# Kernel tuning notes

Measured on AMD Instinct MI355X. Metric: run time of the kernel, lower is better.

The kernel has to match this reference:

```python
import jax, jax.numpy as jnp
import numpy as np

B, Hh, Ww, D = 16, 74, 74, 768   # batch, patch-grid h, patch-grid w, feature dim
NH, NO = 8, 16                    # humans / objects per image
N_REL = 117                       # HOI relation classes


def _make_boxes(key, n):
    # valid boxes: x2 > x1, y2 > y1, all within [0, 74]
    k1, k2, k3, k4 = jax.random.split(key, 4)
    x1 = jax.random.randint(k1, (B, n), 0, Ww - 16)
    y1 = jax.random.randint(k2, (B, n), 0, Hh - 16)
    bw = jax.random.randint(k3, (B, n), 2, 16)
    bh = jax.random.randint(k4, (B, n), 2, 16)
    return jnp.stack([x1, y1, x1 + bw, y1 + bh], axis=-1).astype(jnp.int32)


def setup_inputs() -> dict:
    key = jax.random.key(0)
    ks = jax.random.split(key, 8)
    features = jax.random.normal(ks[0], (B, Hh, Ww, D), dtype=jnp.float32)
    human_boxes = _make_boxes(ks[1], NH)
    obj_boxes = _make_boxes(ks[2], NO)
    s = 0.02
    W1 = jax.random.normal(ks[3], (2 * D, 512), dtype=jnp.float32) * s
    b1 = jnp.zeros((512,), jnp.float32)
    W2 = jax.random.normal(ks[4], (512, 256), dtype=jnp.float32) * s
    b2 = jnp.zeros((256,), jnp.float32)
    W3 = jax.random.normal(ks[5], (256, N_REL), dtype=jnp.float32) * s
    b3 = jnp.zeros((N_REL,), jnp.float32)
    return {"features": features, "human_boxes": human_boxes, "obj_boxes": obj_boxes,
            "W1": W1, "b1": b1, "W2": W2, "b2": b2, "W3": W3, "b3": b3}


def _roi_mean(feats, boxes):
    # feats: [h, w, D]; boxes: [N, 4] int (x1, y1, x2, y2) in patch coords.
    # Mean of feats[y1:y2, x1:x2] via a summed-area table (vectorized, one pass).
    integ = jnp.cumsum(jnp.cumsum(feats, axis=0), axis=1)
    integ = jnp.pad(integ, ((1, 0), (1, 0), (0, 0)))  # [h+1, w+1, D]
    x1, y1, x2, y2 = boxes[:, 0], boxes[:, 1], boxes[:, 2], boxes[:, 3]
    s = integ[y2, x2] - integ[y1, x2] - integ[y2, x1] + integ[y1, x1]  # [N, D]
    area = ((y2 - y1) * (x2 - x1)).astype(feats.dtype)[:, None]
    return s / area


def reference(features, human_boxes, obj_boxes, W1, b1, W2, b2, W3, b3):
    hf = jax.vmap(_roi_mean)(features, human_boxes)  # [B, NH, D]
    of = jax.vmap(_roi_mean)(features, obj_boxes)    # [B, NO, D]
    # pairwise concat: for every (human, object) pair -> [B, NH, NO, 2D]
    pairs = jnp.concatenate([
        jnp.broadcast_to(hf[:, :, None, :], (B, NH, NO, D)),
        jnp.broadcast_to(of[:, None, :, :], (B, NH, NO, D)),
    ], axis=-1).reshape(B * NH * NO, 2 * D)
    h = jax.nn.relu(pairs @ W1 + b1)
    h = jax.nn.relu(h @ W2 + b2)
    return h @ W3 + b3  # [B*NH*NO, 117] relation scores
```

## Files before the change

kernel.cpp:

```cpp
#include <hip/hip_runtime.h>

#define BB   16
#define HH   74
#define WW   74
#define DD   768
#define NHh  8
#define NOo  16
#define NREL 117
#define NKQ  8
#define KCH  96
#define ABSTRIDE (384 * 512)

#define FMA4(A, s, W) \
    A.x = fmaf((s), (W).x, A.x); A.y = fmaf((s), (W).y, A.y); \
    A.z = fmaf((s), (W).z, A.z); A.w = fmaf((s), (W).w, A.w);


__global__ __launch_bounds__(512, 6) void roi_gemm1_kernel(const float* __restrict__ feats,
                                                           const int* __restrict__ hboxes,
                                                           const int* __restrict__ oboxes,
                                                           const float* __restrict__ W1,
                                                           float* __restrict__ AB)
{
    __shared__ __align__(16) float part[15][4][KCH];
    __shared__ __align__(16) float xs[4][KCH];
    __shared__ __align__(16) float red[2][4][512];
    int r0 = blockIdx.x * 4;
    int kq = blockIdx.y;
    int t = threadIdx.x;

    if (t < 360) {
        int c4 = t % 24;
        int s  = t / 24;
        for (int r = 0; r < 4; ++r) {
            int row = r0 + r;
            const int* box = (row < 128) ? (hboxes + row * 4) : (oboxes + (row - 128) * 4);
            int x1 = box[0], y1 = box[1], x2 = box[2], y2 = box[3];
            if (s < y2 - y1) {
                int b = (row < 128) ? (row >> 3) : ((row - 128) >> 4);
                int y = y1 + s;
                const float4* rp = (const float4*)(feats + (size_t)((b * HH + y) * WW) * DD + kq * KCH) + c4;
                float4 a0 = make_float4(0.f, 0.f, 0.f, 0.f);
                float4 a1 = make_float4(0.f, 0.f, 0.f, 0.f);
                float4 a2 = make_float4(0.f, 0.f, 0.f, 0.f);
                float4 a3 = make_float4(0.f, 0.f, 0.f, 0.f);
                int x = x1;
                for (; x + 3 < x2; x += 4) {
                    float4 v0 = rp[(size_t)(x + 0) * 192];
                    float4 v1 = rp[(size_t)(x + 1) * 192];
                    float4 v2 = rp[(size_t)(x + 2) * 192];
                    float4 v3 = rp[(size_t)(x + 3) * 192];
                    a0.x += v0.x; a0.y += v0.y; a0.z += v0.z; a0.w += v0.w;
                    a1.x += v1.x; a1.y += v1.y; a1.z += v1.z; a1.w += v1.w;
                    a2.x += v2.x; a2.y += v2.y; a2.z += v2.z; a2.w += v2.w;
                    a3.x += v3.x; a3.y += v3.y; a3.z += v3.z; a3.w += v3.w;
                }
                for (; x < x2; ++x) {
                    float4 v0 = rp[(size_t)x * 192];
                    a0.x += v0.x; a0.y += v0.y; a0.z += v0.z; a0.w += v0.w;
                }
                a0.x += a1.x + a2.x + a3.x;
                a0.y += a1.y + a2.y + a3.y;
                a0.z += a1.z + a2.z + a3.z;
                a0.w += a1.w + a2.w + a3.w;
                *(float4*)&part[s][r][c4 * 4] = a0;
            }
        }
    }
    __syncthreads();

    for (int idx = t; idx < 4 * KCH; idx += 512) {
        int r = idx / KCH;
        int k = idx - r * KCH;
        int row = r0 + r;
        const int* box = (row < 128) ? (hboxes + row * 4) : (oboxes + (row - 128) * 4);
        int bh = box[3] - box[1];
        float inv_area = 1.0f / (float)(bh * (box[2] - box[0]));
        float ssum = 0.f;
        for (int s = 0; s < bh; ++s) ssum += part[s][r][k];
        xs[r][k] = ssum * inv_area;
    }
    __syncthreads();

    if (t < 256) {
        int c  = t & 127;
        int kh = t >> 7;
        int kb = kh * 48;
        const float* W1p = W1 + ((size_t)(((r0 < 128) ? 0 : DD) + kq * KCH + kb)) * 512 + 4 * c;

        float4 a[4];
#pragma unroll
        for (int r = 0; r < 4; ++r) a[r] = make_float4(0.f, 0.f, 0.f, 0.f);

        for (int kk = 0; kk < 48; kk += 8) {
            float4 w[8];
#pragma unroll
            for (int u = 0; u < 8; ++u) w[u] = *(const float4*)(W1p + (size_t)(kk + u) * 512);
#pragma unroll
            for (int r = 0; r < 4; ++r) {
                float4 x0 = *(const float4*)&xs[r][kb + kk];
                float4 x1 = *(const float4*)&xs[r][kb + kk + 4];
                float xv[8] = {x0.x, x0.y, x0.z, x0.w, x1.x, x1.y, x1.z, x1.w};
#pragma unroll
                for (int u = 0; u < 8; ++u) { FMA4(a[r], xv[u], w[u]); }
            }
        }
#pragma unroll
        for (int r = 0; r < 4; ++r) *(float4*)&red[kh][r][4 * c] = a[r];
    }
    __syncthreads();

    float* ABq = AB + (size_t)kq * ABSTRIDE;
    for (int idx = t; idx < 4 * 512; idx += 512) {
        int r = idx >> 9;
        int cc = idx & 511;
        ABq[(size_t)(r0 + r) * 512 + cc] = red[0][r][cc] + red[1][r][cc];
    }
}

__global__ __launch_bounds__(1024, 4) void mlp_kernel(const float* __restrict__ AB,
                                                      const float* __restrict__ b1,
                                                      const float* __restrict__ W2,
                                                      const float* __restrict__ b2,
                                                      const float* __restrict__ W3,
                                                      const float* __restrict__ b3,
                                                      float* __restrict__ out)
{
    __shared__ __align__(16) float h1[8][512];
    __shared__ __align__(16) float red[8][8][256];
    __shared__ __align__(16) float h2[8][256];
    int p0 = blockIdx.x * 8;
    int t = threadIdx.x;

    {
        int r  = t >> 7;
        int k4 = t & 127;
        int p = p0 + r;
        int rowA = p >> 4;
        int rowB = 128 + (p >> 7) * 16 + (p & 15);
        float4 v = ((const float4*)b1)[k4];
#pragma unroll
        for (int q = 0; q < NKQ; ++q) {
            float4 av = ((const float4*)(AB + (size_t)q * ABSTRIDE + (size_t)rowA * 512))[k4];
            float4 bv = ((const float4*)(AB + (size_t)q * ABSTRIDE + (size_t)rowB * 512))[k4];
            v.x += av.x + bv.x; v.y += av.y + bv.y;
            v.z += av.z + bv.z; v.w += av.w + bv.w;
        }
        v.x = v.x > 0.f ? v.x : 0.f; v.y = v.y > 0.f ? v.y : 0.f;
        v.z = v.z > 0.f ? v.z : 0.f; v.w = v.w > 0.f ? v.w : 0.f;
        *(float4*)&h1[r][k4 * 4] = v;
    }
    __syncthreads();

    {
        int c   = t & 63;
        int kq2 = (t >> 6) & 7;
        int rh  = t >> 9;
        int kbase = kq2 * 64;
        const float* W2p = W2 + (size_t)kbase * 256 + 4 * c;
        float4 a[4];
#pragma unroll
        for (int r = 0; r < 4; ++r) a[r] = make_float4(0.f, 0.f, 0.f, 0.f);

        for (int kk = 0; kk < 64; kk += 8) {
            float4 w[8];
#pragma unroll
            for (int u = 0; u < 8; ++u) w[u] = *(const float4*)(W2p + (size_t)(kk + u) * 256);
#pragma unroll
            for (int r = 0; r < 4; ++r) {
                float4 x0 = *(const float4*)&h1[rh * 4 + r][kbase + kk];
                float4 x1 = *(const float4*)&h1[rh * 4 + r][kbase + kk + 4];
                float xv[8] = {x0.x, x0.y, x0.z, x0.w, x1.x, x1.y, x1.z, x1.w};
#pragma unroll
                for (int u = 0; u < 8; ++u) { FMA4(a[r], xv[u], w[u]); }
            }
        }
#pragma unroll
        for (int r = 0; r < 4; ++r) *(float4*)&red[kq2][rh * 4 + r][4 * c] = a[r];
    }
    __syncthreads();

    for (int idx = t; idx < 8 * 256; idx += 1024) {
        int r = idx >> 8;
        int cc = idx & 255;
        float s = b2[cc];
#pragma unroll
        for (int q = 0; q < 8; ++q) s += red[q][r][cc];
        h2[r][cc] = s > 0.f ? s : 0.f;
    }
    __syncthreads();

    float* pr = &red[0][0][0];
    if (t < 8 * NREL) {
        int o = t % NREL;
        int jq = t / NREL;
        float acc[8] = {};
        const float* W3p = W3 + o;
        for (int j = jq * 32; j < jq * 32 + 32; j += 8) {
            float w[8];
#pragma unroll
            for (int u = 0; u < 8; ++u) w[u] = W3p[(size_t)(j + u) * NREL];
#pragma unroll
            for (int r = 0; r < 8; ++r) {
                float4 x0 = *(const float4*)&h2[r][j];
                float4 x1 = *(const float4*)&h2[r][j + 4];
                acc[r] = fmaf(x0.x, w[0], acc[r]); acc[r] = fmaf(x0.y, w[1], acc[r]);
                acc[r] = fmaf(x0.z, w[2], acc[r]); acc[r] = fmaf(x0.w, w[3], acc[r]);
                acc[r] = fmaf(x1.x, w[4], acc[r]); acc[r] = fmaf(x1.y, w[5], acc[r]);
                acc[r] = fmaf(x1.z, w[6], acc[r]); acc[r] = fmaf(x1.w, w[7], acc[r]);
            }
        }
#pragma unroll
        for (int r = 0; r < 8; ++r) pr[(jq * 8 + r) * NREL + o] = acc[r];
    }
    __syncthreads();

    if (t < 8 * NREL) {
        int r = t / NREL;
        int o = t - r * NREL;
        float s = b3[o];
#pragma unroll
        for (int q = 0; q < 8; ++q) s += pr[(q * 8 + r) * NREL + o];
        out[(size_t)(p0 + r) * NREL + o] = s;
    }
}

extern "C" void kernel_launch(void* const* d_in, const int* in_sizes, int n_in,
                              void* d_out, int out_size, void* d_ws, size_t ws_size,
                              hipStream_t stream) {
    const float* feats  = (const float*)d_in[0];
    const int*   hboxes = (const int*)d_in[1];
    const int*   oboxes = (const int*)d_in[2];
    const float* W1     = (const float*)d_in[3];
    const float* b1     = (const float*)d_in[4];
    const float* W2     = (const float*)d_in[5];
    const float* b2     = (const float*)d_in[6];
    const float* W3     = (const float*)d_in[7];
    const float* b3     = (const float*)d_in[8];
    float* out = (float*)d_out;

    float* AB = (float*)d_ws;

    roi_gemm1_kernel<<<dim3(96, NKQ), dim3(512), 0, stream>>>(feats, hboxes, oboxes, W1, AB);
    mlp_kernel<<<dim3(256), dim3(1024), 0, stream>>>(AB, b1, W2, b2, W3, b3, out);
}
```

Measured before the change: 43.84 us.

## Split ROI mean and first GEMM into separate kernels, halve K-split count

The fused ROI-pooling plus first-layer GEMM kernel becomes two kernels. A row-mean kernel has one block per box read all 768 features per pixel and write pooled rows to workspace. A GEMM kernel then multiplies those rows by W1. The K split drops from 8 chunks of 96 to 4 chunks of 192, with all 512 threads doing the GEMM and a 4-way reduction in shared memory. This aims for better-coalesced feature reads, fewer partial sums for the MLP kernel to combine, and better thread use. The cost is an extra kernel launch and a workspace round trip for the pooled features.

```diff
diff --git a/kernel.cpp b/kernel.cpp
--- a/kernel.cpp
+++ b/kernel.cpp
@@ -7,8 +7,8 @@
 #define NHh  8
 #define NOo  16
 #define NREL 117
-#define NKQ  8
-#define KCH  96
+#define NKQ  4
+#define KCH  192
 #define ABSTRIDE (384 * 512)
 
 #define FMA4(A, s, W) \
@@ -16,105 +16,109 @@
     A.z = fmaf((s), (W).z, A.z); A.w = fmaf((s), (W).w, A.w);
 
 
-__global__ __launch_bounds__(512, 6) void roi_gemm1_kernel(const float* __restrict__ feats,
-                                                           const int* __restrict__ hboxes,
-                                                           const int* __restrict__ oboxes,
-                                                           const float* __restrict__ W1,
-                                                           float* __restrict__ AB)
+__global__ __launch_bounds__(768) void rowmean_kernel(const float* __restrict__ feats,
+                                                      const int* __restrict__ hboxes,
+                                                      const int* __restrict__ oboxes,
+                                                      float* __restrict__ X)
 {
-    __shared__ __align__(16) float part[15][4][KCH];
+    __shared__ __align__(16) float part[4][768];
+    int row = blockIdx.x;
+    const int* box = (row < 128) ? (hboxes + row * 4) : (oboxes + (row - 128) * 4);
+    int x1 = box[0], y1 = box[1], x2 = box[2], y2 = box[3];
+    int b = (row < 128) ? (row >> 3) : ((row - 128) >> 4);
+    int t = threadIdx.x;
+    int c4 = t % 192;
+    int s  = t / 192;
+
+    float4 a0 = make_float4(0.f, 0.f, 0.f, 0.f);
+    float4 a1 = make_float4(0.f, 0.f, 0.f, 0.f);
+    float4 a2 = make_float4(0.f, 0.f, 0.f, 0.f);
+    float4 a3 = make_float4(0.f, 0.f, 0.f, 0.f);
+    for (int y = y1 + s; y < y2; y += 4) {
+        const float4* rp = (const float4*)(feats + (size_t)((b * HH + y) * WW) * DD) + c4;
+        int x = x1;
+        for (; x + 3 < x2; x += 4) {
+            float4 v0 = rp[(size_t)(x + 0) * 192];
+            float4 v1 = rp[(size_t)(x + 1) * 192];
+            float4 v2 = rp[(size_t)(x + 2) * 192];
+            float4 v3 = rp[(size_t)(x + 3) * 192];
+            a0.x += v0.x; a0.y += v0.y; a0.z += v0.z; a0.w += v0.w;
+            a1.x += v1.x; a1.y += v1.y; a1.z += v1.z; a1.w += v1.w;
+            a2.x += v2.x; a2.y += v2.y; a2.z += v2.z; a2.w += v2.w;
+            a3.x += v3.x; a3.y += v3.y; a3.z += v3.z; a3.w += v3.w;
+        }
+        for (; x < x2; ++x) {
+            float4 v0 = rp[(size_t)x * 192];
+            a0.x += v0.x; a0.y += v0.y; a0.z += v0.z; a0.w += v0.w;
+        }
+    }
+    a0.x += a1.x + a2.x + a3.x;
+    a0.y += a1.y + a2.y + a3.y;
+    a0.z += a1.z + a2.z + a3.z;
+    a0.w += a1.w + a2.w + a3.w;
+    *(float4*)&part[s][c4 * 4] = a0;
+    __syncthreads();
+
+    float inv_area = 1.0f / (float)((y2 - y1) * (x2 - x1));
+    float v = (part[0][t] + part[1][t] + part[2][t] + part[3][t]) * inv_area;
+    X[(size_t)row * DD + t] = v;
+}
+
+__global__ __launch_bounds__(512) void gemm1_kernel(const float* __restrict__ X,
+                                                    const float* __restrict__ W1,
+                                                    float* __restrict__ AB)
+{
     __shared__ __align__(16) float xs[4][KCH];
-    __shared__ __align__(16) float red[2][4][512];
+    __shared__ __align__(16) float red[4][4][512];
     int r0 = blockIdx.x * 4;
     int kq = blockIdx.y;
     int t = threadIdx.x;
 
-    if (t < 360) {
-        int c4 = t % 24;
-        int s  = t / 24;
-        for (int r = 0; r < 4; ++r) {
-            int row = r0 + r;
-            const int* box = (row < 128) ? (hboxes + row * 4) : (oboxes + (row - 128) * 4);
-            int x1 = box[0], y1 = box[1], x2 = box[2], y2 = box[3];
-            if (s < y2 - y1) {
-                int b = (row < 128) ? (row >> 3) : ((row - 128) >> 4);
-                int y = y1 + s;
-                const float4* rp = (const float4*)(feats + (size_t)((b * HH + y) * WW) * DD + kq * KCH) + c4;
-                float4 a0 = make_float4(0.f, 0.f, 0.f, 0.f);
-                float4 a1 = make_float4(0.f, 0.f, 0.f, 0.f);
-                float4 a2 = make_float4(0.f, 0.f, 0.f, 0.f);
-                float4 a3 = make_float4(0.f, 0.f, 0.f, 0.f);
-                int x = x1;
-                for (; x + 3 < x2; x += 4) {
-                    float4 v0 = rp[(size_t)(x + 0) * 192];
-                    float4 v1 = rp[(size_t)(x + 1) * 192];
-                    float4 v2 = rp[(size_t)(x + 2) * 192];
-                    float4 v3 = rp[(size_t)(x + 3) * 192];
-                    a0.x += v0.x; a0.y += v0.y; a0.z += v0.z; a0.w += v0.w;
-                    a1.x += v1.x; a1.y += v1.y; a1.z += v1.z; a1.w += v1.w;
-                    a2.x += v2.x; a2.y += v2.y; a2.z += v2.z; a2.w += v2.w;
-                    a3.x += v3.x; a3.y += v3.y; a3.z += v3.z; a3.w += v3.w;
-                }
-                for (; x < x2; ++x) {
-                    float4 v0 = rp[(size_t)x * 192];
-                    a0.x += v0.x; a0.y += v0.y; a0.z += v0.z; a0.w += v0.w;
-                }
-                a0.x += a1.x + a2.x + a3.x;
-                a0.y += a1.y + a2.y + a3.y;
-                a0.z += a1.z + a2.z + a3.z;
-                a0.w += a1.w + a2.w + a3.w;
-                *(float4*)&part[s][r][c4 * 4] = a0;
-            }
-        }
-    }
-    __syncthreads();
-
-    for (int idx = t; idx < 4 * KCH; idx += 512) {
+    {
+        int r = t / KCH;
+        int k = t - r * KCH;
+        xs[r][k] = X[(size_t)(r0 + r) * DD + kq * KCH + k];
+    }
+    if (t < 256) {
+        int idx = t + 512;
         int r = idx / KCH;
         int k = idx - r * KCH;
-        int row = r0 + r;
-        const int* box = (row < 128) ? (hboxes + row * 4) : (oboxes + (row - 128) * 4);
-        int bh = box[3] - box[1];
-        float inv_area = 1.0f / (float)(bh * (box[2] - box[0]));
-        float ssum = 0.f;
-        for (int s = 0; s < bh; ++s) ssum += part[s][r][k];
-        xs[r][k] = ssum * inv_area;
-    }
-    __syncthreads();
-
-    if (t < 256) {
-        int c  = t & 127;
-        int kh = t >> 7;
-        int kb = kh * 48;
-        const float* W1p = W1 + ((size_t)(((r0 < 128) ? 0 : DD) + kq * KCH + kb)) * 512 + 4 * c;
-
-        float4 a[4];
-#pragma unroll
-        for (int r = 0; r < 4; ++r) a[r] = make_float4(0.f, 0.f, 0.f, 0.f);
-
-        for (int kk = 0; kk < 48; kk += 8) {
-            float4 w[8];
-#pragma unroll
-            for (int u = 0; u < 8; ++u) w[u] = *(const float4*)(W1p + (size_t)(kk + u) * 512);
-#pragma unroll
-            for (int r = 0; r < 4; ++r) {
-                float4 x0 = *(const float4*)&xs[r][kb + kk];
-                float4 x1 = *(const float4*)&xs[r][kb + kk + 4];
-                float xv[8] = {x0.x, x0.y, x0.z, x0.w, x1.x, x1.y, x1.z, x1.w};
-#pragma unroll
-                for (int u = 0; u < 8; ++u) { FMA4(a[r], xv[u], w[u]); }
-            }
-        }
-#pragma unroll
-        for (int r = 0; r < 4; ++r) *(float4*)&red[kh][r][4 * c] = a[r];
-    }
+        xs[r][k] = X[(size_t)(r0 + r) * DD + kq * KCH + k];
+    }
+    __syncthreads();
+
+    int c  = t & 127;
+    int kh = t >> 7;
+    int kb = kh * 48;
+    const float* W1p = W1 + ((size_t)(((r0 < 128) ? 0 : DD) + kq * KCH + kb)) * 512 + 4 * c;
+
+    float4 a[4];
+#pragma unroll
+    for (int r = 0; r < 4; ++r) a[r] = make_float4(0.f, 0.f, 0.f, 0.f);
+
+    for (int kk = 0; kk < 48; kk += 8) {
+        float4 w[8];
+#pragma unroll
+        for (int u = 0; u < 8; ++u) w[u] = *(const float4*)(W1p + (size_t)(kk + u) * 512);
+#pragma unroll
+        for (int r = 0; r < 4; ++r) {
+            float4 x0 = *(const float4*)&xs[r][kb + kk];
+            float4 x1 = *(const float4*)&xs[r][kb + kk + 4];
+            float xv[8] = {x0.x, x0.y, x0.z, x0.w, x1.x, x1.y, x1.z, x1.w};
+#pragma unroll
+            for (int u = 0; u < 8; ++u) { FMA4(a[r], xv[u], w[u]); }
+        }
+    }
+#pragma unroll
+    for (int r = 0; r < 4; ++r) *(float4*)&red[kh][r][4 * c] = a[r];
     __syncthreads();
 
     float* ABq = AB + (size_t)kq * ABSTRIDE;
     for (int idx = t; idx < 4 * 512; idx += 512) {
         int r = idx >> 9;
         int cc = idx & 511;
-        ABq[(size_t)(r0 + r) * 512 + cc] = red[0][r][cc] + red[1][r][cc];
+        ABq[(size_t)(r0 + r) * 512 + cc] = red[0][r][cc] + red[1][r][cc]
+                                         + red[2][r][cc] + red[3][r][cc];
     }
 }
 
@@ -240,7 +244,9 @@
     float* out = (float*)d_out;
 
     float* AB = (float*)d_ws;
-
-    roi_gemm1_kernel<<<dim3(96, NKQ), dim3(512), 0, stream>>>(feats, hboxes, oboxes, W1, AB);
+    float* X  = AB + (size_t)NKQ * ABSTRIDE;
+
+    rowmean_kernel<<<dim3(384), dim3(768), 0, stream>>>(feats, hboxes, oboxes, X);
+    gemm1_kernel<<<dim3(96, NKQ), dim3(512), 0, stream>>>(X, W1, AB);
     mlp_kernel<<<dim3(256), dim3(1024), 0, stream>>>(AB, b1, W2, b2, W3, b3, out);
 }
```

Result: slower. 49.64 us (+13.3%).

## Process one ROI row per block instead of four in ROI+GEMM1 kernel

Applied to the files above, without the earlier changes.

The fused ROI-mean and first-layer GEMM kernel now handles one box row per block, launching 384×8 blocks instead of 96×8. The GEMM phase uses all 512 threads with a 4-way split over K instead of 256 threads, and the partial sums are reduced from four slices. The aim is more parallelism and better load balance across CUs for the memory-bound box sums. In exchange, each W1 slice is reloaded once per row instead of once per four rows, which raises W1 traffic about fourfold.

```diff
diff --git a/kernel.cpp b/kernel.cpp
--- a/kernel.cpp
+++ b/kernel.cpp
@@ -16,106 +16,89 @@
     A.z = fmaf((s), (W).z, A.z); A.w = fmaf((s), (W).w, A.w);
 
 
-__global__ __launch_bounds__(512, 6) void roi_gemm1_kernel(const float* __restrict__ feats,
-                                                           const int* __restrict__ hboxes,
-                                                           const int* __restrict__ oboxes,
-                                                           const float* __restrict__ W1,
-                                                           float* __restrict__ AB)
+__global__ __launch_bounds__(512) void roi_gemm1_kernel(const float* __restrict__ feats,
+                                                        const int* __restrict__ hboxes,
+                                                        const int* __restrict__ oboxes,
+                                                        const float* __restrict__ W1,
+                                                        float* __restrict__ AB)
 {
-    __shared__ __align__(16) float part[15][4][KCH];
-    __shared__ __align__(16) float xs[4][KCH];
-    __shared__ __align__(16) float red[2][4][512];
-    int r0 = blockIdx.x * 4;
-    int kq = blockIdx.y;
+    __shared__ __align__(16) float part[15][KCH];
+    __shared__ __align__(16) float xs[KCH];
+    __shared__ __align__(16) float red[4][512];
+    int row = blockIdx.x;
+    int kq  = blockIdx.y;
     int t = threadIdx.x;
+
+    const int* box = (row < 128) ? (hboxes + row * 4) : (oboxes + (row - 128) * 4);
+    int x1 = box[0], y1 = box[1], x2 = box[2], y2 = box[3];
+    int bh = y2 - y1;
+    int b = (row < 128) ? (row >> 3) : ((row - 128) >> 4);
 
     if (t < 360) {
         int c4 = t % 24;
         int s  = t / 24;
-        for (int r = 0; r < 4; ++r) {
-            int row = r0 + r;
-            const int* box = (row < 128) ? (hboxes + row * 4) : (oboxes + (row - 128) * 4);
-            int x1 = box[0], y1 = box[1], x2 = box[2], y2 = box[3];
-            if (s < y2 - y1) {
-                int b = (row < 128) ? (row >> 3) : ((row - 128) >> 4);
-                int y = y1 + s;
-                const float4* rp = (const float4*)(feats + (size_t)((b * HH + y) * WW) * DD + kq * KCH) + c4;
-                float4 a0 = make_float4(0.f, 0.f, 0.f, 0.f);
-                float4 a1 = make_float4(0.f, 0.f, 0.f, 0.f);
-                float4 a2 = make_float4(0.f, 0.f, 0.f, 0.f);
-                float4 a3 = make_float4(0.f, 0.f, 0.f, 0.f);
-                int x = x1;
-                for (; x + 3 < x2; x += 4) {
-                    float4 v0 = rp[(size_t)(x + 0) * 192];
-                    float4 v1 = rp[(size_t)(x + 1) * 192];
-                    float4 v2 = rp[(size_t)(x + 2) * 192];
-                    float4 v3 = rp[(size_t)(x + 3) * 192];
-                    a0.x += v0.x; a0.y += v0.y; a0.z += v0.z; a0.w += v0.w;
-                    a1.x += v1.x; a1.y += v1.y; a1.z += v1.z; a1.w += v1.w;
-                    a2.x += v2.x; a2.y += v2.y; a2.z += v2.z; a2.w += v2.w;
-                    a3.x += v3.x; a3.y += v3.y; a3.z += v3.z; a3.w += v3.w;
-                }
-                for (; x < x2; ++x) {
-                    float4 v0 = rp[(size_t)x * 192];
-                    a0.x += v0.x; a0.y += v0.y; a0.z += v0.z; a0.w += v0.w;
-                }
-                a0.x += a1.x + a2.x + a3.x;
-                a0.y += a1.y + a2.y + a3.y;
-                a0.z += a1.z + a2.z + a3.z;
-                a0.w += a1.w + a2.w + a3.w;
-                *(float4*)&part[s][r][c4 * 4] = a0;
-            }
-        }
-    }
-    __syncthreads();
-
-    for (int idx = t; idx < 4 * KCH; idx += 512) {
-        int r = idx / KCH;
-        int k = idx - r * KCH;
-        int row = r0 + r;
-        const int* box = (row < 128) ? (hboxes + row * 4) : (oboxes + (row - 128) * 4);
-        int bh = box[3] - box[1];
-        float inv_area = 1.0f / (float)(bh * (box[2] - box[0]));
+        if (s < bh) {
+            int y = y1 + s;
+            const float4* rp = (const float4*)(feats + (size_t)((b * HH + y) * WW) * DD + kq * KCH) + c4;
+            float4 a0 = make_float4(0.f, 0.f, 0.f, 0.f);
+            float4 a1 = make_float4(0.f, 0.f, 0.f, 0.f);
+            float4 a2 = make_float4(0.f, 0.f, 0.f, 0.f);
+            float4 a3 = make_float4(0.f, 0.f, 0.f, 0.f);
+            int x = x1;
+            for (; x + 3 < x2; x += 4) {
+                float4 v0 = rp[(size_t)(x + 0) * 192];
+                float4 v1 = rp[(size_t)(x + 1) * 192];
+                float4 v2 = rp[(size_t)(x + 2) * 192];
+                float4 v3 = rp[(size_t)(x + 3) * 192];
+                a0.x += v0.x; a0.y += v0.y; a0.z += v0.z; a0.w += v0.w;
+                a1.x += v1.x; a1.y += v1.y; a1.z += v1.z; a1.w += v1.w;
+                a2.x += v2.x; a2.y += v2.y; a2.z += v2.z; a2.w += v2.w;
+                a3.x += v3.x; a3.y += v3.y; a3.z += v3.z; a3.w += v3.w;
+            }
+            for (; x < x2; ++x) {
+                float4 v0 = rp[(size_t)x * 192];
+                a0.x += v0.x; a0.y += v0.y; a0.z += v0.z; a0.w += v0.w;
+            }
+            a0.x += a1.x + a2.x + a3.x;
+            a0.y += a1.y + a2.y + a3.y;
+            a0.z += a1.z + a2.z + a3.z;
+            a0.w += a1.w + a2.w + a3.w;
+            *(float4*)&part[s][c4 * 4] = a0;
+        }
+    }
+    __syncthreads();
+
+    if (t < KCH) {
+        float inv_area = 1.0f / (float)(bh * (x2 - x1));
         float ssum = 0.f;
-        for (int s = 0; s < bh; ++s) ssum += part[s][r][k];
-        xs[r][k] = ssum * inv_area;
-    }
-    __syncthreads();
-
-    if (t < 256) {
+        for (int s = 0; s < bh; ++s) ssum += part[s][t];
+        xs[t] = ssum * inv_area;
+    }
+    __syncthreads();
+
+    {
         int c  = t & 127;
         int kh = t >> 7;
-        int kb = kh * 48;
-        const float* W1p = W1 + ((size_t)(((r0 < 128) ? 0 : DD) + kq * KCH + kb)) * 512 + 4 * c;
-
-        float4 a[4];
-#pragma unroll
-        for (int r = 0; r < 4; ++r) a[r] = make_float4(0.f, 0.f, 0.f, 0.f);
-
-        for (int kk = 0; kk < 48; kk += 8) {
+        int kb = kh * 24;
+        const float* W1p = W1 + ((size_t)(((row < 128) ? 0 : DD) + kq * KCH + kb)) * 512 + 4 * c;
+
+        float4 a = make_float4(0.f, 0.f, 0.f, 0.f);
+        for (int kk = 0; kk < 24; kk += 8) {
             float4 w[8];
 #pragma unroll
             for (int u = 0; u < 8; ++u) w[u] = *(const float4*)(W1p + (size_t)(kk + u) * 512);
-#pragma unroll
-            for (int r = 0; r < 4; ++r) {
-                float4 x0 = *(const float4*)&xs[r][kb + kk];
-                float4 x1 = *(const float4*)&xs[r][kb + kk + 4];
-                float xv[8] = {x0.x, x0.y, x0.z, x0.w, x1.x, x1.y, x1.z, x1.w};
-#pragma unroll
-                for (int u = 0; u < 8; ++u) { FMA4(a[r], xv[u], w[u]); }
-            }
-        }
-#pragma unroll
-        for (int r = 0; r < 4; ++r) *(float4*)&red[kh][r][4 * c] = a[r];
+            float4 x0 = *(const float4*)&xs[kb + kk];
+            float4 x1v = *(const float4*)&xs[kb + kk + 4];
+            float xv[8] = {x0.x, x0.y, x0.z, x0.w, x1v.x, x1v.y, x1v.z, x1v.w};
+#pragma unroll
+            for (int u = 0; u < 8; ++u) { FMA4(a, xv[u], w[u]); }
+        }
+        *(float4*)&red[kh][4 * c] = a;
     }
     __syncthreads();
 
     float* ABq = AB + (size_t)kq * ABSTRIDE;
-    for (int idx = t; idx < 4 * 512; idx += 512) {
-        int r = idx >> 9;
-        int cc = idx & 511;
-        ABq[(size_t)(r0 + r) * 512 + cc] = red[0][r][cc] + red[1][r][cc];
-    }
+    ABq[(size_t)row * 512 + t] = red[0][t] + red[1][t] + red[2][t] + red[3][t];
 }
 
 __global__ __launch_bounds__(1024, 4) void mlp_kernel(const float* __restrict__ AB,
@@ -241,6 +224,6 @@
 
     float* AB = (float*)d_ws;
 
-    roi_gemm1_kernel<<<dim3(96, NKQ), dim3(512), 0, stream>>>(feats, hboxes, oboxes, W1, AB);
+    roi_gemm1_kernel<<<dim3(384, NKQ), dim3(512), 0, stream>>>(feats, hboxes, oboxes, W1, AB);
     mlp_kernel<<<dim3(256), dim3(1024), 0, stream>>>(AB, b1, W2, b2, W3, b3, out);
 }
```

Result: slower. 53.27 us (+21.5%).

## Split ROI row summation into a separate wide-grid kernel before GEMM1

Applied to the files above, without the earlier changes.

Moves the per-box-row feature summation out of the fused ROI+GEMM1 kernel into a dedicated kernel with one block per (box row, y offset), each covering the full 768-wide feature vector. The GEMM1 kernel then reads the partial row sums from a workspace buffer and reduces them over box height. This is meant to raise parallelism and make the feature reads more contiguous than the old layout, where 360 threads per block each read 96-channel slices. The cost is an extra kernel launch plus a round trip of partial sums through global memory, and many early-exiting blocks for short boxes.

```diff
diff --git a/kernel.cpp b/kernel.cpp
--- a/kernel.cpp
+++ b/kernel.cpp
@@ -9,6 +9,7 @@
 #define NREL 117
 #define NKQ  8
 #define KCH  96
+#define MAXBH 15
 #define ABSTRIDE (384 * 512)
 
 #define FMA4(A, s, W) \
@@ -16,69 +17,71 @@
     A.z = fmaf((s), (W).z, A.z); A.w = fmaf((s), (W).w, A.w);
 
 
-__global__ __launch_bounds__(512, 6) void roi_gemm1_kernel(const float* __restrict__ feats,
-                                                           const int* __restrict__ hboxes,
-                                                           const int* __restrict__ oboxes,
-                                                           const float* __restrict__ W1,
-                                                           float* __restrict__ AB)
+__global__ __launch_bounds__(192) void roi_rows_kernel(const float* __restrict__ feats,
+                                                       const int* __restrict__ hboxes,
+                                                       const int* __restrict__ oboxes,
+                                                       float* __restrict__ P)
 {
-    __shared__ __align__(16) float part[15][4][KCH];
+    int row = blockIdx.x;
+    int q   = blockIdx.y;
+    const int* box = (row < 128) ? (hboxes + row * 4) : (oboxes + (row - 128) * 4);
+    int x1 = box[0], y1 = box[1], x2 = box[2], y2 = box[3];
+    if (q >= y2 - y1) return;
+    int b = (row < 128) ? (row >> 3) : ((row - 128) >> 4);
+    int y = y1 + q;
+
+    int t = threadIdx.x;
+    const float4* rp = (const float4*)(feats + (size_t)((b * HH + y) * WW) * DD) + t;
+
+    float4 a0 = make_float4(0.f, 0.f, 0.f, 0.f);
+    float4 a1 = make_float4(0.f, 0.f, 0.f, 0.f);
+    float4 a2 = make_float4(0.f, 0.f, 0.f, 0.f);
+    float4 a3 = make_float4(0.f, 0.f, 0.f, 0.f);
+    int x = x1;
+    for (; x + 3 < x2; x += 4) {
+        float4 v0 = rp[(size_t)(x + 0) * 192];
+        float4 v1 = rp[(size_t)(x + 1) * 192];
+        float4 v2 = rp[(size_t)(x + 2) * 192];
+        float4 v3 = rp[(size_t)(x + 3) * 192];
+        a0.x += v0.x; a0.y += v0.y; a0.z += v0.z; a0.w += v0.w;
+        a1.x += v1.x; a1.y += v1.y; a1.z += v1.z; a1.w += v1.w;
+        a2.x += v2.x; a2.y += v2.y; a2.z += v2.z; a2.w += v2.w;
+        a3.x += v3.x; a3.y += v3.y; a3.z += v3.z; a3.w += v3.w;
+    }
+    for (; x < x2; ++x) {
+        float4 v0 = rp[(size_t)x * 192];
+        a0.x += v0.x; a0.y += v0.y; a0.z += v0.z; a0.w += v0.w;
+    }
+    a0.x += a1.x + a2.x + a3.x;
+    a0.y += a1.y + a2.y + a3.y;
+    a0.z += a1.z + a2.z + a3.z;
+    a0.w += a1.w + a2.w + a3.w;
+    ((float4*)(P + (size_t)(row * MAXBH + q) * DD))[t] = a0;
+}
+
+__global__ __launch_bounds__(512) void gemm1_kernel(const float* __restrict__ P,
+                                                    const int* __restrict__ hboxes,
+                                                    const int* __restrict__ oboxes,
+                                                    const float* __restrict__ W1,
+                                                    float* __restrict__ AB)
+{
     __shared__ __align__(16) float xs[4][KCH];
     __shared__ __align__(16) float red[2][4][512];
     int r0 = blockIdx.x * 4;
     int kq = blockIdx.y;
     int t = threadIdx.x;
 
-    if (t < 360) {
-        int c4 = t % 24;
-        int s  = t / 24;
-        for (int r = 0; r < 4; ++r) {
-            int row = r0 + r;
-            const int* box = (row < 128) ? (hboxes + row * 4) : (oboxes + (row - 128) * 4);
-            int x1 = box[0], y1 = box[1], x2 = box[2], y2 = box[3];
-            if (s < y2 - y1) {
-                int b = (row < 128) ? (row >> 3) : ((row - 128) >> 4);
-                int y = y1 + s;
-                const float4* rp = (const float4*)(feats + (size_t)((b * HH + y) * WW) * DD + kq * KCH) + c4;
-                float4 a0 = make_float4(0.f, 0.f, 0.f, 0.f);
-                float4 a1 = make_float4(0.f, 0.f, 0.f, 0.f);
-                float4 a2 = make_float4(0.f, 0.f, 0.f, 0.f);
-                float4 a3 = make_float4(0.f, 0.f, 0.f, 0.f);
-                int x = x1;
-                for (; x + 3 < x2; x += 4) {
-                    float4 v0 = rp[(size_t)(x + 0) * 192];
-                    float4 v1 = rp[(size_t)(x + 1) * 192];
-                    float4 v2 = rp[(size_t)(x + 2) * 192];
-                    float4 v3 = rp[(size_t)(x + 3) * 192];
-                    a0.x += v0.x; a0.y += v0.y; a0.z += v0.z; a0.w += v0.w;
-                    a1.x += v1.x; a1.y += v1.y; a1.z += v1.z; a1.w += v1.w;
-                    a2.x += v2.x; a2.y += v2.y; a2.z += v2.z; a2.w += v2.w;
-                    a3.x += v3.x; a3.y += v3.y; a3.z += v3.z; a3.w += v3.w;
-                }
-                for (; x < x2; ++x) {
-                    float4 v0 = rp[(size_t)x * 192];
-                    a0.x += v0.x; a0.y += v0.y; a0.z += v0.z; a0.w += v0.w;
-                }
-                a0.x += a1.x + a2.x + a3.x;
-                a0.y += a1.y + a2.y + a3.y;
-                a0.z += a1.z + a2.z + a3.z;
-                a0.w += a1.w + a2.w + a3.w;
-                *(float4*)&part[s][r][c4 * 4] = a0;
-            }
-        }
-    }
-    __syncthreads();
-
-    for (int idx = t; idx < 4 * KCH; idx += 512) {
-        int r = idx / KCH;
-        int k = idx - r * KCH;
+    if (t < 4 * KCH) {
+        int r = t / KCH;
+        int k = t - r * KCH;
         int row = r0 + r;
         const int* box = (row < 128) ? (hboxes + row * 4) : (oboxes + (row - 128) * 4);
         int bh = box[3] - box[1];
         float inv_area = 1.0f / (float)(bh * (box[2] - box[0]));
-        float ssum = 0.f;
-        for (int s = 0; s < bh; ++s) ssum += part[s][r][k];
-        xs[r][k] = ssum * inv_area;
+        const float* Pp = P + (size_t)(row * MAXBH) * DD + kq * KCH + k;
+        float s = 0.f;
+        for (int yy = 0; yy < bh; ++yy) s += Pp[(size_t)yy * DD];
+        xs[r][k] = s * inv_area;
     }
     __syncthreads();
 
@@ -239,8 +242,10 @@
     const float* b3     = (const float*)d_in[8];
     float* out = (float*)d_out;
 
-    float* AB = (float*)d_ws;
-
-    roi_gemm1_kernel<<<dim3(96, NKQ), dim3(512), 0, stream>>>(feats, hboxes, oboxes, W1, AB);
+    float* P  = (float*)d_ws;
+    float* AB = P + (size_t)384 * MAXBH * DD;
+
+    roi_rows_kernel<<<dim3(384, MAXBH), dim3(192), 0, stream>>>(feats, hboxes, oboxes, P);
+    gemm1_kernel<<<dim3(96, NKQ), dim3(512), 0, stream>>>(P, hboxes, oboxes, W1, AB);
     mlp_kernel<<<dim3(256), dim3(1024), 0, stream>>>(AB, b1, W2, b2, W3, b3, out);
 }
```

Result: slower. 57.80 us (+31.8%).
